# Optimization experiments

Hardware: AMD Instinct MI355X
Metric: run time of the kernel (lower is better)

The kernel has to match this reference:

```python
import jax, jax.numpy as jnp
import numpy as np

SCALES = [3, 5, 7, 9]


def _conv1d(x, w, b, k):
    # x: (BN, 1, L), w: (1, 1, k), b: (1,) -> (BN, 1, L), 'same' padding (k//2)
    y = jax.lax.conv_general_dilated(
        x, w, window_strides=(1,), padding=[(k // 2, k // 2)],
        dimension_numbers=("NCH", "OIH", "NCH"))
    return y + b[None, :, None]


def setup_inputs() -> dict:
    key = jax.random.key(0)
    ks = jax.random.split(key, 16)
    B, N, L = 64, 321, 720
    inp = {"x": jax.random.normal(ks[0], (B, N, L), dtype=jnp.float32)}
    # Conv1d(1,1,k) params, kaiming-ish scale 1/sqrt(k)
    for i, s in enumerate(SCALES):
        inp[f"cw{i}"] = jax.random.normal(ks[1 + 2 * i], (1, 1, s), dtype=jnp.float32) / np.sqrt(s)
        inp[f"cb{i}"] = jax.random.normal(ks[2 + 2 * i], (1,), dtype=jnp.float32) * 0.01
    # weight_net: Linear(4,32) -> ReLU -> Linear(32,4) -> Softmax
    inp["W1"] = jax.random.normal(ks[10], (4, 32), dtype=jnp.float32) / np.sqrt(4.0)
    inp["b1"] = jnp.zeros((32,), dtype=jnp.float32)
    inp["W2"] = jax.random.normal(ks[11], (32, 4), dtype=jnp.float32) / np.sqrt(32.0)
    inp["b2"] = jnp.zeros((4,), dtype=jnp.float32)
    return inp


def reference(x, cw0, cb0, cw1, cb1, cw2, cb2, cw3, cb3, W1, b1, W2, b2):
    B, N, L = x.shape
    xf = x.reshape(B * N, 1, L)
    cparams = [(cw0, cb0), (cw1, cb1), (cw2, cb2), (cw3, cb3)]
    feats, ents = [], []
    for (w, b), k in zip(cparams, SCALES):
        f = _conv1d(xf, w, b, k)                      # (BN, 1, L)
        prob = jax.nn.softmax(f, axis=-1)
        ent = -(prob * jnp.log(prob + 1e-8)).sum(axis=-1)  # (BN, 1)
        feats.append(f)
        ents.append(ent)
    entropy_vec = jnp.concatenate(ents, axis=-1)      # (BN, 4)
    h = jax.nn.relu(entropy_vec @ W1 + b1)
    weights = jax.nn.softmax(h @ W2 + b2, axis=-1)    # (BN, 4)
    stacked = jnp.stack(feats, axis=1)                # (BN, 4, 1, L)
    trend = (stacked * weights[:, :, None, None]).sum(axis=1)  # (BN, 1, L)
    return trend.reshape(B, N, L)
```

## Files before the change

### kernel.cpp

```cpp
#include <hip/hip_runtime.h>
#include <math.h>

#define NT 64
#define L_LEN 720
#define NROWS (64 * 321)

#define LOG2E 1.4426950408889634f
#define LN2   0.6931471805599453f

typedef float f32x2 __attribute__((ext_vector_type(2)));

__device__ __forceinline__ f32x2 pkfma(f32x2 a, f32x2 b, f32x2 c) {
    return __builtin_elementwise_fma(a, b, c);
}

__device__ __forceinline__ float rfl(float v) {
    return __int_as_float(__builtin_amdgcn_readfirstlane(__float_as_int(v)));
}

template<int CTRL, int RM>
__device__ __forceinline__ float dpp_add(float x) {
    int t = __builtin_amdgcn_update_dpp(0, __float_as_int(x), CTRL, RM, 0xf, true);
    return x + __int_as_float(t);
}

__device__ __forceinline__ float wave_sum64(float x) {
    x = dpp_add<0x111, 0xf>(x);
    x = dpp_add<0x112, 0xf>(x);
    x = dpp_add<0x114, 0xf>(x);
    x = dpp_add<0x118, 0xf>(x);
    x = dpp_add<0x142, 0xa>(x);
    x = dpp_add<0x143, 0xc>(x);
    return __int_as_float(__builtin_amdgcn_readlane(__float_as_int(x), 63));
}

__device__ __forceinline__ float half_sum32(float x) {
    x = dpp_add<0x111, 0xf>(x);
    x = dpp_add<0x112, 0xf>(x);
    x = dpp_add<0x114, 0xf>(x);
    x = dpp_add<0x118, 0xf>(x);
    x = dpp_add<0x142, 0xa>(x);
    return __int_as_float(__builtin_amdgcn_readlane(__float_as_int(x), 31));
}

__global__ __launch_bounds__(NT, 4) void trend_kernel(
    const float* __restrict__ x,
    const float* __restrict__ cw0, const float* __restrict__ cb0,
    const float* __restrict__ cw1, const float* __restrict__ cb1,
    const float* __restrict__ cw2, const float* __restrict__ cb2,
    const float* __restrict__ cw3, const float* __restrict__ cb3,
    const float* __restrict__ W1, const float* __restrict__ b1,
    const float* __restrict__ W2, const float* __restrict__ b2,
    float* __restrict__ out)
{
    const int lane = threadIdx.x;
    const int row  = blockIdx.x;

    const float* __restrict__ xr = x + (size_t)row * L_LEN;

    const int ll = (lane < 60) ? lane : 59;
    const int e0 = 12 * ll - 4;
    float xw[20];
#pragma unroll
    for (int q = 0; q < 5; ++q) {
        int e = e0 + 4 * q;
        e = (e < 0) ? 0 : ((e > L_LEN - 4) ? (L_LEN - 4) : e);
        float4 v = *(const float4*)(xr + e);
        xw[4 * q + 0] = v.x; xw[4 * q + 1] = v.y;
        xw[4 * q + 2] = v.z; xw[4 * q + 3] = v.w;
    }

    const float* cws[4] = {cw0, cw1, cw2, cw3};
    const float* cbs[4] = {cb0, cb1, cb2, cb3};
    float w2[4][9], bs2[4];
#pragma unroll
    for (int s = 0; s < 4; ++s) {
        const int k = 3 + 2 * s;
        bs2[s] = rfl(cbs[s][0] * LOG2E);
#pragma unroll
        for (int t = 0; t < 9; ++t)
            w2[s][t] = (t < k) ? rfl(cws[s][t] * LOG2E) : 0.0f;
    }

    if (lane == 0)  { xw[0] = 0.f; xw[1] = 0.f; xw[2] = 0.f; xw[3] = 0.f; }
    if (lane == 59) { xw[16] = 0.f; xw[17] = 0.f; xw[18] = 0.f; xw[19] = 0.f; }

#pragma unroll
    for (int t = 0; t < 20; ++t) asm volatile("" : "+v"(xw[t]));

    f32x2 p[14];
#pragma unroll
    for (int i = 0; i < 14; ++i) p[i] = (f32x2){xw[i], xw[i + 6]};

    f32x2 fu[4][6];
    f32x2 Spk[4] = {{0.f,0.f},{0.f,0.f},{0.f,0.f},{0.f,0.f}};
    f32x2 Tpk[4] = {{0.f,0.f},{0.f,0.f},{0.f,0.f},{0.f,0.f}};
#pragma unroll
    for (int j = 0; j < 6; ++j) {
#pragma unroll
        for (int s = 0; s < 4; ++s) {
            const int k = 3 + 2 * s;
            const int off = 3 - s;
            f32x2 u = (f32x2){bs2[s], bs2[s]};
#pragma unroll
            for (int t = 0; t < k; ++t) {
                const f32x2 wv = (f32x2){w2[s][t], w2[s][t]};
                u = pkfma(wv, p[j + off + t], u);
            }
            fu[s][j] = u;
            f32x2 ev;
            ev.x = __builtin_amdgcn_exp2f(u.x);
            ev.y = __builtin_amdgcn_exp2f(u.y);
            Spk[s] += ev;
            Tpk[s] = pkfma(u, ev, Tpk[s]);
        }
    }

#pragma unroll
    for (int s = 0; s < 4; ++s)
#pragma unroll
        for (int j = 0; j < 6; ++j) {
            asm volatile("" : "+v"(fu[s][j].x));
            asm volatile("" : "+v"(fu[s][j].y));
        }

    const bool active = lane < 60;
    float S[4], Tu[4];
#pragma unroll
    for (int s = 0; s < 4; ++s) {
        S[s]  = active ? (Spk[s].x + Spk[s].y) : 0.0f;
        Tu[s] = active ? (Tpk[s].x + Tpk[s].y) : 0.0f;
    }

    float ent[4];
#pragma unroll
    for (int s = 0; s < 4; ++s) {
        float Sg = wave_sum64(S[s]);
        float Tg = wave_sum64(Tu[s]);
        ent[s] = LN2 * (__builtin_amdgcn_logf(Sg)
                        - Tg * __builtin_amdgcn_rcpf(Sg));
    }

    const int hidx = lane & 31;
    float h = b1[hidx];
#pragma unroll
    for (int s = 0; s < 4; ++s) h = fmaf(ent[s], W1[s * 32 + hidx], h);
    h = fmaxf(h, 0.0f);

    const float4 w2v = ((const float4*)W2)[hidx];
    float lg0 = half_sum32(h * w2v.x) + b2[0];
    float lg1 = half_sum32(h * w2v.y) + b2[1];
    float lg2 = half_sum32(h * w2v.z) + b2[2];
    float lg3 = half_sum32(h * w2v.w) + b2[3];

    float m = fmaxf(fmaxf(lg0, lg1), fmaxf(lg2, lg3));
    float e0w = __expf(lg0 - m), e1w = __expf(lg1 - m);
    float e2w = __expf(lg2 - m), e3w = __expf(lg3 - m);
    float inv = LN2 / (e0w + e1w + e2w + e3w);
    const float wg0 = e0w * inv, wg1 = e1w * inv;
    const float wg2 = e2w * inv, wg3 = e3w * inv;

    if (active) {
        f32x2 o[6];
#pragma unroll
        for (int j = 0; j < 6; ++j) {
            f32x2 acc = (f32x2){wg0, wg0} * fu[0][j];
            acc = pkfma((f32x2){wg1, wg1}, fu[1][j], acc);
            acc = pkfma((f32x2){wg2, wg2}, fu[2][j], acc);
            acc = pkfma((f32x2){wg3, wg3}, fu[3][j], acc);
            o[j] = acc;
        }
        float* __restrict__ orow = out + (size_t)row * L_LEN + 12 * lane;
        float4 v0 = {o[0].x, o[1].x, o[2].x, o[3].x};
        float4 v1 = {o[4].x, o[5].x, o[0].y, o[1].y};
        float4 v2 = {o[2].y, o[3].y, o[4].y, o[5].y};
        *(float4*)(orow)     = v0;
        *(float4*)(orow + 4) = v1;
        *(float4*)(orow + 8) = v2;
    }
}

extern "C" void kernel_launch(void* const* d_in, const int* in_sizes, int n_in,
                              void* d_out, int out_size, void* d_ws, size_t ws_size,
                              hipStream_t stream) {
    const float* xp  = (const float*)d_in[0];
    const float* cw0 = (const float*)d_in[1];
    const float* cb0 = (const float*)d_in[2];
    const float* cw1 = (const float*)d_in[3];
    const float* cb1 = (const float*)d_in[4];
    const float* cw2 = (const float*)d_in[5];
    const float* cb2 = (const float*)d_in[6];
    const float* cw3 = (const float*)d_in[7];
    const float* cb3 = (const float*)d_in[8];
    const float* W1  = (const float*)d_in[9];
    const float* b1  = (const float*)d_in[10];
    const float* W2  = (const float*)d_in[11];
    const float* b2  = (const float*)d_in[12];
    float* outp = (float*)d_out;

    trend_kernel<<<NROWS, NT, 0, stream>>>(xp, cw0, cb0, cw1, cb1, cw2, cb2,
                                           cw3, cb3, W1, b1, W2, b2, outp);
}
```

Baseline: 32.90 us.

## Fold weighted conv outputs into a single merged 9-tap filter

Because the output is a linear combination of four convolutions, the code merges the per-scale taps and biases (scaled by the softmax weights) into one 9-tap filter and recomputes the output from the input window. This avoids keeping the 24 packed per-scale conv results live in registers across the reductions and MLP. The lower register pressure is used to raise the launch-bounds occupancy hint from 4 to 6. The cost is recomputing a 9-tap packed FMA per output, and the merged weights are reduced through readfirstlane.

```diff
diff --git a/kernel.cpp b/kernel.cpp
--- a/kernel.cpp
+++ b/kernel.cpp
@@ -43,7 +43,7 @@
     return __int_as_float(__builtin_amdgcn_readlane(__float_as_int(x), 31));
 }
 
-__global__ __launch_bounds__(NT, 4) void trend_kernel(
+__global__ __launch_bounds__(NT, 6) void trend_kernel(
     const float* __restrict__ x,
     const float* __restrict__ cw0, const float* __restrict__ cb0,
     const float* __restrict__ cw1, const float* __restrict__ cb1,
@@ -85,14 +85,15 @@
     if (lane == 0)  { xw[0] = 0.f; xw[1] = 0.f; xw[2] = 0.f; xw[3] = 0.f; }
     if (lane == 59) { xw[16] = 0.f; xw[17] = 0.f; xw[18] = 0.f; xw[19] = 0.f; }
 
-#pragma unroll
-    for (int t = 0; t < 20; ++t) asm volatile("" : "+v"(xw[t]));
-
     f32x2 p[14];
 #pragma unroll
     for (int i = 0; i < 14; ++i) p[i] = (f32x2){xw[i], xw[i + 6]};
-
-    f32x2 fu[4][6];
+#pragma unroll
+    for (int i = 0; i < 14; ++i) {
+        asm volatile("" : "+v"(p[i].x));
+        asm volatile("" : "+v"(p[i].y));
+    }
+
     f32x2 Spk[4] = {{0.f,0.f},{0.f,0.f},{0.f,0.f},{0.f,0.f}};
     f32x2 Tpk[4] = {{0.f,0.f},{0.f,0.f},{0.f,0.f},{0.f,0.f}};
 #pragma unroll
@@ -107,7 +108,6 @@
                 const f32x2 wv = (f32x2){w2[s][t], w2[s][t]};
                 u = pkfma(wv, p[j + off + t], u);
             }
-            fu[s][j] = u;
             f32x2 ev;
             ev.x = __builtin_amdgcn_exp2f(u.x);
             ev.y = __builtin_amdgcn_exp2f(u.y);
@@ -116,14 +116,6 @@
         }
     }
 
-#pragma unroll
-    for (int s = 0; s < 4; ++s)
-#pragma unroll
-        for (int j = 0; j < 6; ++j) {
-            asm volatile("" : "+v"(fu[s][j].x));
-            asm volatile("" : "+v"(fu[s][j].y));
-        }
-
     const bool active = lane < 60;
     float S[4], Tu[4];
 #pragma unroll
@@ -160,14 +152,32 @@
     const float wg0 = e0w * inv, wg1 = e1w * inv;
     const float wg2 = e2w * inv, wg3 = e3w * inv;
 
+    float Wm[9] = {0,0,0,0,0,0,0,0,0};
+    float Bm = 0.f;
+    {
+        const float wgt[4] = {wg0, wg1, wg2, wg3};
+#pragma unroll
+        for (int s = 0; s < 4; ++s) {
+            const int k = 3 + 2 * s;
+            const int off = 3 - s;
+#pragma unroll
+            for (int t = 0; t < k; ++t)
+                Wm[off + t] = rfl(fmaf(wgt[s], w2[s][t], Wm[off + t]));
+            Bm = fmaf(wgt[s], bs2[s], Bm);
+        }
+        Bm = rfl(Bm);
+    }
+
     if (active) {
         f32x2 o[6];
 #pragma unroll
         for (int j = 0; j < 6; ++j) {
-            f32x2 acc = (f32x2){wg0, wg0} * fu[0][j];
-            acc = pkfma((f32x2){wg1, wg1}, fu[1][j], acc);
-            acc = pkfma((f32x2){wg2, wg2}, fu[2][j], acc);
-            acc = pkfma((f32x2){wg3, wg3}, fu[3][j], acc);
+            f32x2 acc = (f32x2){Bm, Bm};
+#pragma unroll
+            for (int d = 0; d < 9; ++d) {
+                const f32x2 wv = (f32x2){Wm[d], Wm[d]};
+                acc = pkfma(wv, p[j + d], acc);
+            }
             o[j] = acc;
         }
         float* __restrict__ orow = out + (size_t)row * L_LEN + 12 * lane;
```

New measurement: 115.4 us. +250.8%, slower.
